# Optimization experiments

Measured on AMD Instinct MI355X. Metric: run time of the kernel, lower is better.

Reference implementation:

```python
import jax, jax.numpy as jnp
import numpy as np

D_MODEL = 1024
NUM_HEADS = 16
DEPTH = D_MODEL // NUM_HEADS
B, S = 2, 2048


def setup_inputs() -> dict:
    key = jax.random.key(0)
    k1, k2, k3 = jax.random.split(key, 3)
    x = jax.random.normal(k1, (B, S, D_MODEL), dtype=jnp.float32)
    # causal mask: 1.0 where attention is disallowed (upper triangle)
    causal = 1.0 - jnp.tril(jnp.ones((S, S), dtype=jnp.float32))
    mask = causal[None, None, :, :]  # [1,1,S,S]
    w_attn = jax.random.normal(k2, (D_MODEL, 3 * D_MODEL), dtype=jnp.float32) * 0.02
    b_attn = jnp.zeros((3 * D_MODEL,), dtype=jnp.float32)
    w_proj = jax.random.normal(k3, (D_MODEL, D_MODEL), dtype=jnp.float32) * 0.02
    b_proj = jnp.zeros((D_MODEL,), dtype=jnp.float32)
    return {"x": x, "mask": mask, "w_attn": w_attn, "b_attn": b_attn,
            "w_proj": w_proj, "b_proj": b_proj}


def _split_heads(t):
    # [B,S,D] -> [B,H,S,depth]
    b, s, _ = t.shape
    return t.reshape(b, s, NUM_HEADS, DEPTH).transpose(0, 2, 1, 3)


def reference(x, mask, w_attn, b_attn, w_proj, b_proj):
    # QKV projection (Conv1d == pointwise dense over last axis)
    qkv = jnp.einsum('bsd,de->bse', x, w_attn) + b_attn
    q, k, v = jnp.split(qkv, 3, axis=2)
    q, k, v = _split_heads(q), _split_heads(k), _split_heads(v)  # [B,H,S,depth]
    present = jnp.stack([k, v], axis=1)  # [B,2,H,S,depth]
    # scaled dot-product attention (inference: no dropout)
    scores = jnp.einsum('bhqd,bhkd->bhqk', q, k) / jnp.sqrt(
        jnp.asarray(DEPTH, dtype=x.dtype))
    scores = scores + mask * (-1e9)
    attn = jax.nn.softmax(scores, axis=-1)
    out = jnp.einsum('bhqk,bhkd->bhqd', attn, v)
    # merge heads: [B,H,S,depth] -> [B,S,D]
    out = out.transpose(0, 2, 1, 3).reshape(x.shape[0], -1, D_MODEL)
    out = jnp.einsum('bsd,de->bse', out, w_proj) + b_proj
    return out, present
```

## Files before the change

### kernel.cpp

```cpp
#include <hip/hip_runtime.h>
#include <stdint.h>

typedef unsigned short u16;
typedef unsigned int u32;
typedef short bf16x8 __attribute__((ext_vector_type(8)));
typedef float f32x4 __attribute__((ext_vector_type(4)));

#define SEQ 2048
#define NH 16
#define DM 1024
#define DEPTH 64

#define QSCALE 0.18033688f
#define SMAX 16.0f

__device__ __forceinline__ u16 f2bf(float f) {
  union { float f; u32 i; } v; v.f = f;
  u32 x = v.i;
  x += 0x7fffu + ((x >> 16) & 1u);
  return (u16)(x >> 16);
}

__device__ __forceinline__ float fexp2(float x) {
#if __has_builtin(__builtin_amdgcn_exp2f)
  return __builtin_amdgcn_exp2f(x);
#else
  return exp2f(x);
#endif
}

__global__ __launch_bounds__(256)
void cvt_bf16(const float* __restrict__ src, u16* __restrict__ dst) {
  int i = (blockIdx.x * 256 + threadIdx.x) * 4;
  float4 v = *(const float4*)(src + i);
  ushort4 o; o.x = f2bf(v.x); o.y = f2bf(v.y); o.z = f2bf(v.z); o.w = f2bf(v.w);
  *(ushort4*)(dst + i) = o;
}

__global__ __launch_bounds__(256)
void cvtT_bf16(const float* __restrict__ src, u16* __restrict__ dst, int K, int N) {
  __shared__ float t[32][33];
  const int tid = threadIdx.x;
  const int k0 = blockIdx.y << 5, n0 = blockIdx.x << 5;
  {
    int r = tid >> 3, c4 = (tid & 7) << 2;
    float4 v = *(const float4*)(src + (size_t)(k0 + r) * N + n0 + c4);
    t[r][c4 + 0] = v.x; t[r][c4 + 1] = v.y; t[r][c4 + 2] = v.z; t[r][c4 + 3] = v.w;
  }
  __syncthreads();
  {
    int n = tid >> 3, k4 = (tid & 7) << 2;
    ushort4 o;
    o.x = f2bf(t[k4 + 0][n]); o.y = f2bf(t[k4 + 1][n]);
    o.z = f2bf(t[k4 + 2][n]); o.w = f2bf(t[k4 + 3][n]);
    *(ushort4*)(dst + (size_t)(n0 + n) * K + k0 + k4) = o;
  }
}

__global__ __launch_bounds__(256)
void v_transpose(const float* __restrict__ present, u16* __restrict__ vt) {
  __shared__ float t[64][65];
  const int tid = threadIdx.x;
  const int st = blockIdx.x, bh = blockIdx.y;
  const int b = bh >> 4, h = bh & 15;
  const int s0 = st << 6;
  const float* vsrc = present + (((size_t)((b * 2 + 1) * NH + h)) * SEQ + s0) * DEPTH;
  u16* vdst = vt + ((size_t)(b * NH + h) * DEPTH) * SEQ + s0;
#pragma unroll
  for (int i = 0; i < 4; ++i) {
    int e = tid + (i << 8);
    int r = e >> 4, c = e & 15;
    float4 v = *(const float4*)(vsrc + (size_t)r * DEPTH + (c << 2));
    t[r][(c << 2) + 0] = v.x; t[r][(c << 2) + 1] = v.y;
    t[r][(c << 2) + 2] = v.z; t[r][(c << 2) + 3] = v.w;
  }
  __syncthreads();
#pragma unroll
  for (int i = 0; i < 2; ++i) {
    int e = tid + (i << 8);
    int d = e >> 3, s8 = (e & 7) << 3;
    ushort4 o0, o1;
    o0.x = f2bf(t[s8 + 0][d]); o0.y = f2bf(t[s8 + 1][d]);
    o0.z = f2bf(t[s8 + 2][d]); o0.w = f2bf(t[s8 + 3][d]);
    o1.x = f2bf(t[s8 + 4][d]); o1.y = f2bf(t[s8 + 5][d]);
    o1.z = f2bf(t[s8 + 6][d]); o1.w = f2bf(t[s8 + 7][d]);
    *(ushort4*)(vdst + (size_t)d * SEQ + s8) = o0;
    *(ushort4*)(vdst + (size_t)d * SEQ + s8 + 4) = o1;
  }
}

__global__ __launch_bounds__(256)
void gemm_mfma(const u16* __restrict__ A, const u16* __restrict__ Bt,
               const float* __restrict__ bias, int M, int N, int K, int mode,
               float* __restrict__ outf, u16* __restrict__ qws,
               float* __restrict__ present, u16* __restrict__ kbp)
{
  __shared__ __align__(16) u16 As[128][40];
  __shared__ __align__(16) u16 Bs[128][40];
  const int tid = threadIdx.x;
  const int m0 = blockIdx.y << 7;
  const int n0 = blockIdx.x << 7;
  const int w = tid >> 6, lane = tid & 63;
  const int lane15 = lane & 15, quad = lane >> 4;
  const int wm = (w >> 1) << 6, wn = (w & 1) << 6;

  const int r0 = tid >> 2, kq = tid & 3;
  const u16* aptr0 = A  + (size_t)(m0 + r0) * K + kq * 8;
  const u16* aptr1 = A  + (size_t)(m0 + r0 + 64) * K + kq * 8;
  const u16* bptr0 = Bt + (size_t)(n0 + r0) * K + kq * 8;
  const u16* bptr1 = Bt + (size_t)(n0 + r0 + 64) * K + kq * 8;

  f32x4 acc[4][4] = {};

  bf16x8 ra0 = *(const bf16x8*)(aptr0);
  bf16x8 ra1 = *(const bf16x8*)(aptr1);
  bf16x8 rb0 = *(const bf16x8*)(bptr0);
  bf16x8 rb1 = *(const bf16x8*)(bptr1);

  for (int k0 = 0; k0 < K; k0 += 32) {
    *(bf16x8*)&As[r0][kq * 8]      = ra0;
    *(bf16x8*)&As[r0 + 64][kq * 8] = ra1;
    *(bf16x8*)&Bs[r0][kq * 8]      = rb0;
    *(bf16x8*)&Bs[r0 + 64][kq * 8] = rb1;
    __syncthreads();
    if (k0 + 32 < K) {
      ra0 = *(const bf16x8*)(aptr0 + k0 + 32);
      ra1 = *(const bf16x8*)(aptr1 + k0 + 32);
      rb0 = *(const bf16x8*)(bptr0 + k0 + 32);
      rb1 = *(const bf16x8*)(bptr1 + k0 + 32);
    }
    bf16x8 af[4], bf[4];
#pragma unroll
    for (int tm = 0; tm < 4; ++tm)
      af[tm] = *(const bf16x8*)&As[wm + tm * 16 + lane15][quad * 8];
#pragma unroll
    for (int tn = 0; tn < 4; ++tn)
      bf[tn] = *(const bf16x8*)&Bs[wn + tn * 16 + lane15][quad * 8];
#pragma unroll
    for (int tm = 0; tm < 4; ++tm)
#pragma unroll
      for (int tn = 0; tn < 4; ++tn)
        acc[tm][tn] = __builtin_amdgcn_mfma_f32_16x16x32_bf16(af[tm], bf[tn], acc[tm][tn], 0, 0, 0);
    __syncthreads();
  }

#pragma unroll
  for (int tn = 0; tn < 4; ++tn) {
    const int c = n0 + wn + tn * 16 + lane15;
    const float bc = bias[c];
    const int t = c >> 10, cc = c & 1023;
    const int h = cc >> 6, d = cc & 63;
#pragma unroll
    for (int tm = 0; tm < 4; ++tm) {
#pragma unroll
      for (int r = 0; r < 4; ++r) {
        const int m = m0 + wm + tm * 16 + quad * 4 + r;
        const float val = acc[tm][tn][r] + bc;
        if (mode == 1) {
          outf[(size_t)m * N + c] = val;
        } else {
          const int b = m >> 11, s = m & 2047;
          if (t == 0) {
            qws[(((size_t)(b * NH + h) * SEQ) + s) * DEPTH + d] = f2bf(val * QSCALE);
          } else {
            const size_t pidx = (((size_t)((b * 2 + (t - 1)) * NH + h) * SEQ) + s) * DEPTH + d;
            present[pidx] = val;
            if (t == 1)
              kbp[(((size_t)(b * NH + h) * SEQ) + s) * DEPTH + d] = f2bf(val);
          }
        }
      }
    }
  }
}

__global__ __launch_bounds__(256)
void attn_mfma(const u16* __restrict__ qb, const u16* __restrict__ kb,
               const u16* __restrict__ vt, u16* __restrict__ attnb)
{
  __shared__ __align__(16) u16 Qs[64][72];
  __shared__ __align__(16) u16 Ks[64][72];
  __shared__ __align__(16) u16 VsT[64][72];
  __shared__ __align__(16) u16 Ps[64][72];

  const int tid = threadIdx.x;
  const int w = tid >> 6, lane = tid & 63;
  const int lane15 = lane & 15, quad = lane >> 4;
  const int p = blockIdx.x, bh = blockIdx.y;
  const int b = bh >> 4, h = bh & 15;

  const u16* qbh = qb + ((size_t)(b * NH + h) * SEQ) * DEPTH;
  const u16* kbh = kb + ((size_t)(b * NH + h) * SEQ) * DEPTH;
  const u16* vbh = vt + ((size_t)(b * NH + h) * DEPTH) * SEQ;

  bf16x8 ones;
#pragma unroll
  for (int j = 0; j < 8; ++j) ones[j] = (short)0x3F80;

  const int u0 = tid, u1 = tid + 256;
  u16* ksd0 = &Ks[u0 >> 3][(u0 & 7) << 3];
  u16* ksd1 = &Ks[u1 >> 3][(u1 & 7) << 3];
  u16* vsd0 = &VsT[u0 >> 3][(u0 & 7) << 3];
  u16* vsd1 = &VsT[u1 >> 3][(u1 & 7) << 3];
  const size_t voff0 = (size_t)(u0 >> 3) * SEQ + ((u0 & 7) << 3);
  const size_t voff1 = (size_t)(u1 >> 3) * SEQ + ((u1 & 7) << 3);

#pragma unroll 1
  for (int half = 0; half < 2; ++half) {
    const int tt = half ? (31 - p) : p;
    const int q0 = tt << 6;
    __syncthreads();
#pragma unroll
    for (int i = 0; i < 2; ++i) {
      int e = tid + (i << 8);
      *(bf16x8*)&Qs[e >> 3][(e & 7) << 3] =
          *(const bf16x8*)(qbh + (size_t)q0 * DEPTH + e * 8);
    }
    bf16x8 rk0 = *(const bf16x8*)(kbh + u0 * 8);
    bf16x8 rk1 = *(const bf16x8*)(kbh + u1 * 8);
    bf16x8 rv0 = *(const bf16x8*)(vbh + voff0);
    bf16x8 rv1 = *(const bf16x8*)(vbh + voff1);

    f32x4 accO[4] = {};
    f32x4 accL = {};
    const int qg = q0 + w * 16 + quad * 4;
    bf16x8 aQ0, aQ1;

    const int nchunk = tt + 1;
#pragma unroll 1
    for (int ct = 0; ct < nchunk; ++ct) {
      const int kk0 = ct << 6;
      __syncthreads();
      if (ct == 0) {
        aQ0 = *(const bf16x8*)&Qs[w * 16 + lane15][quad * 8];
        aQ1 = *(const bf16x8*)&Qs[w * 16 + lane15][32 + quad * 8];
      }
      *(bf16x8*)ksd0 = rk0; *(bf16x8*)ksd1 = rk1;
      *(bf16x8*)vsd0 = rv0; *(bf16x8*)vsd1 = rv1;
      __syncthreads();
      if (ct < tt) {
        const int kn = kk0 + 64;
        rk0 = *(const bf16x8*)(kbh + (size_t)kn * DEPTH + u0 * 8);
        rk1 = *(const bf16x8*)(kbh + (size_t)kn * DEPTH + u1 * 8);
        rv0 = *(const bf16x8*)(vbh + voff0 + kn);
        rv1 = *(const bf16x8*)(vbh + voff1 + kn);
      }
      f32x4 sc[4] = {};
#pragma unroll
      for (int tc = 0; tc < 4; ++tc) {
        bf16x8 bk0 = *(const bf16x8*)&Ks[tc * 16 + lane15][quad * 8];
        bf16x8 bk1 = *(const bf16x8*)&Ks[tc * 16 + lane15][32 + quad * 8];
        sc[tc] = __builtin_amdgcn_mfma_f32_16x16x32_bf16(aQ0, bk0, sc[tc], 0, 0, 0);
        sc[tc] = __builtin_amdgcn_mfma_f32_16x16x32_bf16(aQ1, bk1, sc[tc], 0, 0, 0);
      }
      const bool diag = (ct == tt);
#pragma unroll
      for (int tc = 0; tc < 4; ++tc) {
#pragma unroll
        for (int r = 0; r < 4; ++r) {
          float pe = fexp2(sc[tc][r] - SMAX);
          if (diag) {
            int kg = kk0 + tc * 16 + lane15;
            if (kg > qg + r) pe = 0.f;
          }
          Ps[w * 16 + quad * 4 + r][tc * 16 + lane15] = f2bf(pe);
        }
      }
#pragma unroll
      for (int ks = 0; ks < 2; ++ks) {
        bf16x8 ap = *(const bf16x8*)&Ps[w * 16 + lane15][ks * 32 + quad * 8];
        accL = __builtin_amdgcn_mfma_f32_16x16x32_bf16(ap, ones, accL, 0, 0, 0);
#pragma unroll
        for (int tn = 0; tn < 4; ++tn) {
          bf16x8 bv = *(const bf16x8*)&VsT[tn * 16 + lane15][ks * 32 + quad * 8];
          accO[tn] = __builtin_amdgcn_mfma_f32_16x16x32_bf16(ap, bv, accO[tn], 0, 0, 0);
        }
      }
    }

#pragma unroll
    for (int r = 0; r < 4; ++r) {
      const float li = 1.0f / accL[r];
      u16* obase = attnb + ((size_t)(b * SEQ + qg + r)) * DM + h * DEPTH;
#pragma unroll
      for (int tn = 0; tn < 4; ++tn)
        obase[tn * 16 + lane15] = f2bf(accO[tn][r] * li);
    }
  }
}

extern "C" void kernel_launch(void* const* d_in, const int* in_sizes, int n_in,
                              void* d_out, int out_size, void* d_ws, size_t ws_size,
                              hipStream_t stream) {
  (void)in_sizes; (void)n_in; (void)out_size; (void)ws_size;
  const float* x      = (const float*)d_in[0];
  const float* w_attn = (const float*)d_in[2];
  const float* b_attn = (const float*)d_in[3];
  const float* w_proj = (const float*)d_in[4];
  const float* b_proj = (const float*)d_in[5];

  float* out     = (float*)d_out;
  float* present = out + (size_t)2 * SEQ * DM;

  u16* qws   = (u16*)d_ws;
  u16* kbp   = qws + (size_t)4194304;
  u16* xb    = kbp + (size_t)4194304;
  u16* vtp   = xb;
  u16* wabT  = xb + (size_t)4194304;
  u16* attnb = wabT;
  u16* wpbT  = wabT + (size_t)4194304;

  cvt_bf16<<<4096, 256, 0, stream>>>(x, xb);
  cvtT_bf16<<<dim3(96, 32), 256, 0, stream>>>(w_attn, wabT, DM, 3 * DM);
  cvtT_bf16<<<dim3(32, 32), 256, 0, stream>>>(w_proj, wpbT, DM, DM);

  gemm_mfma<<<dim3(24, 32), 256, 0, stream>>>(xb, wabT, b_attn,
                                              2 * SEQ, 3 * DM, DM, 0,
                                              nullptr, qws, present, kbp);
  v_transpose<<<dim3(32, 32), 256, 0, stream>>>(present, vtp);
  attn_mfma<<<dim3(16, 32), 256, 0, stream>>>(qws, kbp, vtp, attnb);
  gemm_mfma<<<dim3(8, 32), 256, 0, stream>>>(attnb, wpbT, b_proj,
                                             2 * SEQ, DM, DM, 1,
                                             out, nullptr, nullptr, nullptr);
}
```

Before: 219.8 us.

## Use direct global-to-LDS loads in GEMM with K-tile 64, merge weight converts

The GEMM now stages A and B tiles with global_load_lds straight into shared memory, no longer going through registers. It doubles the K tile to 64, so each pass runs two MFMA sub-steps per barrier pair. This drops the register-prefetch overlap and uses an unpadded 64-wide LDS row, which may cause bank conflicts on fragment reads. Separately, the two weight transpose-convert launches are merged into one grid to save a launch.

```diff
diff --git a/kernel.cpp b/kernel.cpp
--- a/kernel.cpp
+++ b/kernel.cpp
@@ -29,6 +29,12 @@
 #endif
 }
 
+__device__ __forceinline__ void gload_lds16(const u16* g, u16* l) {
+  __builtin_amdgcn_global_load_lds(
+      (const __attribute__((address_space(1))) u32*)g,
+      (__attribute__((address_space(3))) u32*)l, 16, 0, 0);
+}
+
 __global__ __launch_bounds__(256)
 void cvt_bf16(const float* __restrict__ src, u16* __restrict__ dst) {
   int i = (blockIdx.x * 256 + threadIdx.x) * 4;
@@ -38,10 +44,16 @@
 }
 
 __global__ __launch_bounds__(256)
-void cvtT_bf16(const float* __restrict__ src, u16* __restrict__ dst, int K, int N) {
+void cvtT_both(const float* __restrict__ wa, const float* __restrict__ wp,
+               u16* __restrict__ dwa, u16* __restrict__ dwp) {
   __shared__ float t[32][33];
   const int tid = threadIdx.x;
-  const int k0 = blockIdx.y << 5, n0 = blockIdx.x << 5;
+  const int bx = blockIdx.x;
+  const float* src; u16* dst; int N, n0;
+  if (bx < 96) { src = wa; dst = dwa; N = 3 * DM; n0 = bx << 5; }
+  else         { src = wp; dst = dwp; N = DM;     n0 = (bx - 96) << 5; }
+  const int k0 = blockIdx.y << 5;
+  const int K = DM;
   {
     int r = tid >> 3, c4 = (tid & 7) << 2;
     float4 v = *(const float4*)(src + (size_t)(k0 + r) * N + n0 + c4);
@@ -95,8 +107,8 @@
                float* __restrict__ outf, u16* __restrict__ qws,
                float* __restrict__ present, u16* __restrict__ kbp)
 {
-  __shared__ __align__(16) u16 As[128][40];
-  __shared__ __align__(16) u16 Bs[128][40];
+  __shared__ __align__(16) u16 As[128][64];
+  __shared__ __align__(16) u16 Bs[128][64];
   const int tid = threadIdx.x;
   const int m0 = blockIdx.y << 7;
   const int n0 = blockIdx.x << 7;
@@ -104,43 +116,35 @@
   const int lane15 = lane & 15, quad = lane >> 4;
   const int wm = (w >> 1) << 6, wn = (w & 1) << 6;
 
-  const int r0 = tid >> 2, kq = tid & 3;
-  const u16* aptr0 = A  + (size_t)(m0 + r0) * K + kq * 8;
-  const u16* aptr1 = A  + (size_t)(m0 + r0 + 64) * K + kq * 8;
-  const u16* bptr0 = Bt + (size_t)(n0 + r0) * K + kq * 8;
-  const u16* bptr1 = Bt + (size_t)(n0 + r0 + 64) * K + kq * 8;
+  const int srow = lane >> 3;
+  const int scol = (lane & 7) << 3;
+  const u16* agbase = A  + (size_t)(m0 + w * 32 + srow) * K + scol;
+  const u16* bgbase = Bt + (size_t)(n0 + w * 32 + srow) * K + scol;
 
   f32x4 acc[4][4] = {};
 
-  bf16x8 ra0 = *(const bf16x8*)(aptr0);
-  bf16x8 ra1 = *(const bf16x8*)(aptr1);
-  bf16x8 rb0 = *(const bf16x8*)(bptr0);
-  bf16x8 rb1 = *(const bf16x8*)(bptr1);
-
-  for (int k0 = 0; k0 < K; k0 += 32) {
-    *(bf16x8*)&As[r0][kq * 8]      = ra0;
-    *(bf16x8*)&As[r0 + 64][kq * 8] = ra1;
-    *(bf16x8*)&Bs[r0][kq * 8]      = rb0;
-    *(bf16x8*)&Bs[r0 + 64][kq * 8] = rb1;
+  for (int k0 = 0; k0 < K; k0 += 64) {
+#pragma unroll
+    for (int i = 0; i < 4; ++i) {
+      gload_lds16(agbase + (size_t)(i * 8) * K + k0, &As[w * 32 + i * 8][0]);
+      gload_lds16(bgbase + (size_t)(i * 8) * K + k0, &Bs[w * 32 + i * 8][0]);
+    }
     __syncthreads();
-    if (k0 + 32 < K) {
-      ra0 = *(const bf16x8*)(aptr0 + k0 + 32);
-      ra1 = *(const bf16x8*)(aptr1 + k0 + 32);
-      rb0 = *(const bf16x8*)(bptr0 + k0 + 32);
-      rb1 = *(const bf16x8*)(bptr1 + k0 + 32);
-    }
-    bf16x8 af[4], bf[4];
-#pragma unroll
-    for (int tm = 0; tm < 4; ++tm)
-      af[tm] = *(const bf16x8*)&As[wm + tm * 16 + lane15][quad * 8];
-#pragma unroll
-    for (int tn = 0; tn < 4; ++tn)
-      bf[tn] = *(const bf16x8*)&Bs[wn + tn * 16 + lane15][quad * 8];
-#pragma unroll
-    for (int tm = 0; tm < 4; ++tm)
+#pragma unroll
+    for (int ks = 0; ks < 2; ++ks) {
+      bf16x8 af[4], bfr[4];
+#pragma unroll
+      for (int tm = 0; tm < 4; ++tm)
+        af[tm] = *(const bf16x8*)&As[wm + tm * 16 + lane15][ks * 32 + quad * 8];
 #pragma unroll
       for (int tn = 0; tn < 4; ++tn)
-        acc[tm][tn] = __builtin_amdgcn_mfma_f32_16x16x32_bf16(af[tm], bf[tn], acc[tm][tn], 0, 0, 0);
+        bfr[tn] = *(const bf16x8*)&Bs[wn + tn * 16 + lane15][ks * 32 + quad * 8];
+#pragma unroll
+      for (int tm = 0; tm < 4; ++tm)
+#pragma unroll
+        for (int tn = 0; tn < 4; ++tn)
+          acc[tm][tn] = __builtin_amdgcn_mfma_f32_16x16x32_bf16(af[tm], bfr[tn], acc[tm][tn], 0, 0, 0);
+    }
     __syncthreads();
   }
 
@@ -311,8 +315,7 @@
   u16* wpbT  = wabT + (size_t)4194304;
 
   cvt_bf16<<<4096, 256, 0, stream>>>(x, xb);
-  cvtT_bf16<<<dim3(96, 32), 256, 0, stream>>>(w_attn, wabT, DM, 3 * DM);
-  cvtT_bf16<<<dim3(32, 32), 256, 0, stream>>>(w_proj, wpbT, DM, DM);
+  cvtT_both<<<dim3(128, 32), 256, 0, stream>>>(w_attn, w_proj, wabT, wpbT);
 
   gemm_mfma<<<dim3(24, 32), 256, 0, stream>>>(xb, wabT, b_attn,
                                               2 * SEQ, 3 * DM, DM, 0,
```

Result: slower. 241.0 us (+9.7%).
